# Optimization experiments

Hardware: AMD Instinct MI355X
Metric: run time of the kernel (lower is better)

Reference implementation:

```python
import jax, jax.numpy as jnp
import numpy as np

D_IN = 2048; D_OUT = 2048; DL = 512; NUM_HEAD = 16; CTX = 2048
HEAD_DIM = D_OUT // NUM_HEAD  # 128


def setup_inputs() -> dict:
    key = jax.random.key(0)
    ks = jax.random.split(key, 20)
    s = 0.02
    def lin(k, din, dout):
        k1, k2 = jax.random.split(k)
        return (jax.random.normal(k1, (din, dout), jnp.float32) * s,
                jax.random.normal(k2, (dout,), jnp.float32) * s)
    w_kv, b_kv = lin(ks[0], D_IN, DL)
    w_ku, b_ku = lin(ks[1], DL, D_OUT // 2)
    w_kr, b_kr = lin(ks[2], D_IN, D_OUT // 2)
    w_vu, b_vu = lin(ks[3], DL, D_OUT)
    w_q,  b_q  = lin(ks[4], D_IN, DL)
    w_qu, b_qu = lin(ks[5], DL, D_OUT // 2)
    w_qr, b_qr = lin(ks[6], DL, D_OUT // 2)
    w_o,  b_o  = lin(ks[7], D_OUT, D_OUT)
    x = jax.random.normal(ks[8], (2, 2048, D_IN), jnp.float32)
    return dict(x=x, w_kv=w_kv, b_kv=b_kv, w_ku=w_ku, b_ku=b_ku, w_kr=w_kr, b_kr=b_kr,
                w_vu=w_vu, b_vu=b_vu, w_q=w_q, b_q=b_q, w_qu=w_qu, b_qu=b_qu,
                w_qr=w_qr, b_qr=b_qr, w_o=w_o, b_o=b_o)


def reference(x, w_kv, b_kv, w_ku, b_ku, w_kr, b_kr, w_vu, b_vu,
              w_q, b_q, w_qu, b_qu, w_qr, b_qr, w_o, b_o):
    b, s, _ = x.shape
    # latent KV compression
    ckv = x @ w_kv + b_kv                                   # (b, s, dl)
    # NOTE: source Rope.forward is a no-op (returns input), replicated faithfully.
    key = jnp.concatenate([ckv @ w_ku + b_ku, x @ w_kr + b_kr], axis=-1)   # (b, s, d_out)
    q_lat = x @ w_q + b_q                                   # (b, s, dl)
    query = jnp.concatenate([q_lat @ w_qu + b_qu, q_lat @ w_qr + b_qr], axis=-1)
    value = ckv @ w_vu + b_vu                               # (b, s, d_out)
    # split heads -> (b, h, s, hd)
    def heads(t):
        return t.reshape(b, s, NUM_HEAD, HEAD_DIM).transpose(0, 2, 1, 3)
    q, k, v = heads(query), heads(key), heads(value)
    scores = jnp.einsum('bhqd,bhkd->bhqk', q, k)
    causal = jnp.tril(jnp.ones((s, s), dtype=bool))
    scores = jnp.where(causal, scores, -jnp.inf)
    at = jax.nn.softmax(scores / jnp.sqrt(jnp.float32(HEAD_DIM)), axis=-1)
    # dropout rate 0 -> identity
    out = jnp.einsum('bhqk,bhkd->bhqd', at, v).transpose(0, 2, 1, 3).reshape(b, s, D_OUT)
    return out @ w_o + b_o
```

## Files before the change

kernel.cpp:

```cpp
#include <hip/hip_runtime.h>
#include <hip/hip_bf16.h>

typedef __hip_bfloat16 bf16;
typedef __bf16 bf16_t;
typedef __bf16 bf16x8 __attribute__((ext_vector_type(8)));
typedef __bf16 bf16x4v __attribute__((ext_vector_type(4)));
typedef float f32x4 __attribute__((ext_vector_type(4)));

#define D_IN 2048
#define D_OUT 2048
#define DL 512
#define NUM_HEAD 16
#define SEQ 2048
#define HEAD_DIM 128
#define BATCH 2
#define NTOK (BATCH * SEQ)
#define SCALE 0.08838834764831845f

struct CTrue  { static constexpr bool value = true;  };
struct CFalse { static constexpr bool value = false; };

__device__ __forceinline__ void stf(float* p, float v) { *p = v; }
__device__ __forceinline__ void stf(bf16_t* p, float v) { *p = (bf16_t)v; }

__device__ __forceinline__ void async_cp16(const bf16_t* g, bf16_t* l) {
    __builtin_amdgcn_global_load_lds(
        (const __attribute__((address_space(1))) void*)g,
        (__attribute__((address_space(3))) void*)l, 16, 0, 0);
}

#define CVTB 8192
#define NTOPS 8

struct TOp { const float* W; bf16_t* Wt; int K, N, nx, nblk; };
struct TOps { TOp op[NTOPS]; };

__global__ __launch_bounds__(256) void prep_kernel(
    const float* __restrict__ x, bf16_t* __restrict__ xb,
    TOps ops,
    const float* __restrict__ b_kv, const float* __restrict__ b_q,
    float* __restrict__ bkvq,
    const float* __restrict__ b_qu, const float* __restrict__ b_qr,
    float* __restrict__ bquqr, int trb)
{
    const int tid = threadIdx.x;
    int blk = blockIdx.x;

    if (blk < CVTB) {
        int i = (blk * 256 + tid) * 4;
        float4 v = *(const float4*)&x[i];
        bf16_t o[4] = {(bf16_t)v.x, (bf16_t)v.y, (bf16_t)v.z, (bf16_t)v.w};
        *(ulong1*)&xb[i] = *(ulong1*)o;
        return;
    }
    blk -= CVTB;
    if (blk < trb) {
        int op = 0;
        while (blk >= ops.op[op].nblk) { blk -= ops.op[op].nblk; ++op; }
        const TOp& t = ops.op[op];
        const int n0 = (blk % t.nx) * 32, k0 = (blk / t.nx) * 32;
        __shared__ float tl[32][33];
        const int c = tid & 31, r0 = tid >> 5;
#pragma unroll
        for (int rr = 0; rr < 32; rr += 8)
            tl[r0 + rr][c] = t.W[(size_t)(k0 + r0 + rr) * t.N + n0 + c];
        __syncthreads();
#pragma unroll
        for (int rr = 0; rr < 32; rr += 8)
            t.Wt[(size_t)(n0 + r0 + rr) * t.K + k0 + c] = (bf16_t)tl[c][r0 + rr];
        return;
    }
    blk -= trb;
    if (blk == 0) {
#pragma unroll
        for (int j = 0; j < 4; ++j) {
            int i = tid + j * 256;
            bkvq[i] = (i < DL) ? b_kv[i] : b_q[i - DL];
        }
    } else {
#pragma unroll
        for (int j = 0; j < 8; ++j) {
            int i = tid + j * 256;
            bquqr[i] = (i < 1024) ? b_qu[i] : b_qr[i - 1024];
        }
    }
}

struct GOp { const bf16_t* A; const bf16_t* Wt; const float* bias;
             void* C; int lda, K, col0, ldc, nx, nblk; float cscale; };
template <int N> struct GOps { GOp op[N]; };

template <typename TC, int NOPS>
__global__ __launch_bounds__(256) void gemm_multi_kernel(GOps<NOPS> ops)
{
    __shared__ __align__(16) bf16_t As[2 * 128 * 32];
    __shared__ __align__(16) bf16_t Bs[2 * 128 * 32];

    int blk = blockIdx.x;
    int opi = 0;
    while (blk >= ops.op[opi].nblk) { blk -= ops.op[opi].nblk; ++opi; }
    const GOp& g = ops.op[opi];

    const int tid  = threadIdx.x;
    const int wave = tid >> 6, lane = tid & 63;
    const int quad = lane >> 4, l16 = lane & 15;
    const int wm = wave & 1, wn = wave >> 1;
    const int m0 = (blk / g.nx) * 128;
    const int n0 = (blk % g.nx) * 128;

    const int r0 = tid >> 2, c0 = (tid & 3) * 8;
    const bf16_t* Ap0 = g.A  + (size_t)(m0 + r0)      * g.lda + c0;
    const bf16_t* Ap1 = g.A  + (size_t)(m0 + r0 + 64) * g.lda + c0;
    const bf16_t* Bp0 = g.Wt + (size_t)(n0 + r0)      * g.K   + c0;
    const bf16_t* Bp1 = g.Wt + (size_t)(n0 + r0 + 64) * g.K   + c0;

    f32x4 acc[4][4];
#pragma unroll
    for (int i = 0; i < 4; ++i)
#pragma unroll
        for (int j = 0; j < 4; ++j) acc[i][j] = (f32x4){0.f, 0.f, 0.f, 0.f};

    for (int k0 = 0; k0 < g.K; k0 += 64) {
        __syncthreads();
#pragma unroll
        for (int p = 0; p < 2; ++p) {
            async_cp16(Ap0 + k0 + p * 32, As + p * 4096 + tid * 8);
            async_cp16(Ap1 + k0 + p * 32, As + p * 4096 + 2048 + tid * 8);
            async_cp16(Bp0 + k0 + p * 32, Bs + p * 4096 + tid * 8);
            async_cp16(Bp1 + k0 + p * 32, Bs + p * 4096 + 2048 + tid * 8);
        }
        __syncthreads();

#pragma unroll
        for (int p = 0; p < 2; ++p) {
            bf16x8 af[4], bfr[4];
#pragma unroll
            for (int t = 0; t < 4; ++t) {
                af[t]  = *(const bf16x8*)&As[p * 4096 + (wm * 64 + t * 16 + l16) * 32 + quad * 8];
                bfr[t] = *(const bf16x8*)&Bs[p * 4096 + (wn * 64 + t * 16 + l16) * 32 + quad * 8];
            }
#pragma unroll
            for (int mt = 0; mt < 4; ++mt)
#pragma unroll
                for (int nt = 0; nt < 4; ++nt)
                    acc[mt][nt] = __builtin_amdgcn_mfma_f32_16x16x32_bf16(
                        af[mt], bfr[nt], acc[mt][nt], 0, 0, 0);
        }
    }

    TC* C = (TC*)g.C;
    const int mrow = m0 + wm * 64 + quad * 4;
#pragma unroll
    for (int mt = 0; mt < 4; ++mt)
#pragma unroll
        for (int nt = 0; nt < 4; ++nt) {
            int col = n0 + wn * 64 + nt * 16 + l16;
            float bv = g.bias[col];
#pragma unroll
            for (int r = 0; r < 4; ++r)
                stf(&C[(size_t)(mrow + mt * 16 + r) * g.ldc + g.col0 + col],
                    (acc[mt][nt][r] + bv) * g.cscale);
        }
}

#define KS_LD 136
#define VT_LD 72
#define KS_SZ (64 * KS_LD)
#define VT_SZ (128 * VT_LD)

__global__ __launch_bounds__(256, 2) void attn_mfma_kernel(
    bf16_t* __restrict__ Qg, const bf16_t* __restrict__ Kg,
    const bf16_t* __restrict__ Vg)
{
    __shared__ __align__(16) bf16_t Ks[2][KS_SZ];
    __shared__ __align__(16) bf16_t Vt[2][VT_SZ];

    const int tid  = threadIdx.x;
    const int wave = tid >> 6;
    const int lane = tid & 63;
    const int quad = lane >> 4;
    const int l16  = lane & 15;

    const int grp = blockIdx.x & 31;
    const int h   = grp & 15;
    const int b   = grp >> 4;
    const int p   = blockIdx.x >> 5;
    const int qtA = p, qtB = 31 - p;
    const int ntiles = qtB + 1;

    const int base = b * SEQ;
    const int hd0  = h * HEAD_DIM;

    bf16x8 qfA[4], qfB[4];
    {
        const bf16_t* qa = Qg + (size_t)(base + qtA * 64 + wave * 16 + l16) * D_OUT + hd0;
        const bf16_t* qb = Qg + (size_t)(base + qtB * 64 + wave * 16 + l16) * D_OUT + hd0;
#pragma unroll
        for (int kb = 0; kb < 4; ++kb) {
            qfA[kb] = *(const bf16x8*)(qa + kb * 32 + quad * 8);
            qfB[kb] = *(const bf16x8*)(qb + kb * 32 + quad * 8);
        }
    }

    f32x4 oA[8], oB[8];
#pragma unroll
    for (int ob = 0; ob < 8; ++ob) {
        oA[ob] = (f32x4){0.f, 0.f, 0.f, 0.f};
        oB[ob] = (f32x4){0.f, 0.f, 0.f, 0.f};
    }
    float lA = 0.f, lB = 0.f;

    const int rk = tid >> 4, ck = (tid & 15) * 8;
    const int kg = (tid & 15) * 4, dg = tid >> 4;
    const int rbase = (rk >> 2) * 8 + (rk & 3);

    bf16x8 kpre[4], vpre[4];
    auto issue = [&](int k0) {
        const bf16_t* kp = Kg + (size_t)(base + k0 + rbase) * D_OUT + hd0 + ck;
        kpre[0] = *(const bf16x8*)(kp);
        kpre[1] = *(const bf16x8*)(kp + (size_t)4  * D_OUT);
        kpre[2] = *(const bf16x8*)(kp + (size_t)32 * D_OUT);
        kpre[3] = *(const bf16x8*)(kp + (size_t)36 * D_OUT);
#pragma unroll
        for (int kk = 0; kk < 4; ++kk)
            vpre[kk] = *(const bf16x8*)&Vg[(size_t)(base + k0 + kg + kk) * D_OUT + hd0 + dg * 8];
    };

    auto stage = [&](int buf) {
        bf16_t* ks = Ks[buf]; bf16_t* vt = Vt[buf];
#pragma unroll
        for (int jj = 0; jj < 4; ++jj)
            *(bf16x8*)&ks[(rk + 16 * jj) * KS_LD + ck] = kpre[jj];
#pragma unroll
        for (int j = 0; j < 8; ++j) {
            bf16x4v pk = {vpre[0][j], vpre[1][j], vpre[2][j], vpre[3][j]};
            *(bf16x4v*)&vt[(dg * 8 + j) * VT_LD + kg] = pk;
        }
    };

    const int qabsA = qtA * 64 + wave * 16 + l16;
    const int qabsB = qtB * 64 + wave * 16 + l16;
    const int qwavA = qtA * 64 + wave * 16;
    const int qwavB = qtB * 64 + wave * 16;

    auto softmax_one = [&](f32x4* s, float& l_i, bf16x8& pb0, bf16x8& pb1) {
#pragma unroll
        for (int nb = 0; nb < 4; ++nb)
#pragma unroll
            for (int r = 0; r < 4; ++r) s[nb][r] = __expf(s[nb][r]);
        float r0 = ((s[0][0] + s[0][1]) + (s[0][2] + s[0][3]))
                 + ((s[1][0] + s[1][1]) + (s[1][2] + s[1][3]));
        float r1 = ((s[2][0] + s[2][1]) + (s[2][2] + s[2][3]))
                 + ((s[3][0] + s[3][1]) + (s[3][2] + s[3][3]));
        l_i += r0 + r1;
#pragma unroll
        for (int r = 0; r < 4; ++r) {
            pb0[r]     = (bf16_t)s[0][r];
            pb0[4 + r] = (bf16_t)s[1][r];
            pb1[r]     = (bf16_t)s[2][r];
            pb1[4 + r] = (bf16_t)s[3][r];
        }
    };

    auto tile_body = [&](auto doa, int cur, int k0) {
        constexpr bool DOA = decltype(doa)::value;
        const bf16_t* ks = Ks[cur];
        const bf16_t* vt = Vt[cur];

        f32x4 sB[4], sA[4];
#pragma unroll
        for (int nb = 0; nb < 4; ++nb) {
            sB[nb] = (f32x4){0.f, 0.f, 0.f, 0.f};
            sA[nb] = (f32x4){0.f, 0.f, 0.f, 0.f};
        }

        __builtin_amdgcn_s_setprio(1);
#pragma unroll
        for (int kb = 0; kb < 4; ++kb)
#pragma unroll
            for (int nb = 0; nb < 4; ++nb) {
                bf16x8 kf = *(const bf16x8*)&ks[(nb * 16 + l16) * KS_LD + kb * 32 + quad * 8];
                sB[nb] = __builtin_amdgcn_mfma_f32_16x16x32_bf16(kf, qfB[kb], sB[nb], 0, 0, 0);
                if constexpr (DOA)
                    sA[nb] = __builtin_amdgcn_mfma_f32_16x16x32_bf16(kf, qfA[kb], sA[nb], 0, 0, 0);
            }
        __builtin_amdgcn_s_setprio(0);

        if (k0 + 63 > qwavB) {
#pragma unroll
            for (int nb = 0; nb < 4; ++nb) {
                int key = k0 + (nb >> 1) * 32 + quad * 8 + (nb & 1) * 4;
#pragma unroll
                for (int r = 0; r < 4; ++r)
                    if (key + r > qabsB) sB[nb][r] = -INFINITY;
            }
        }
        if constexpr (DOA) {
            if (k0 + 63 > qwavA) {
#pragma unroll
                for (int nb = 0; nb < 4; ++nb) {
                    int key = k0 + (nb >> 1) * 32 + quad * 8 + (nb & 1) * 4;
#pragma unroll
                    for (int r = 0; r < 4; ++r)
                        if (key + r > qabsA) sA[nb][r] = -INFINITY;
                }
            }
        }

        bf16x8 pbB0, pbB1, pbA0, pbA1;
        softmax_one(sB, lB, pbB0, pbB1);
        if constexpr (DOA) softmax_one(sA, lA, pbA0, pbA1);

        __builtin_amdgcn_s_setprio(1);
#pragma unroll
        for (int ob = 0; ob < 8; ++ob) {
            bf16x8 v0 = *(const bf16x8*)&vt[(ob * 16 + l16) * VT_LD + quad * 8];
            oB[ob] = __builtin_amdgcn_mfma_f32_16x16x32_bf16(v0, pbB0, oB[ob], 0, 0, 0);
            if constexpr (DOA)
                oA[ob] = __builtin_amdgcn_mfma_f32_16x16x32_bf16(v0, pbA0, oA[ob], 0, 0, 0);
            bf16x8 v1 = *(const bf16x8*)&vt[(ob * 16 + l16) * VT_LD + 32 + quad * 8];
            oB[ob] = __builtin_amdgcn_mfma_f32_16x16x32_bf16(v1, pbB1, oB[ob], 0, 0, 0);
            if constexpr (DOA)
                oA[ob] = __builtin_amdgcn_mfma_f32_16x16x32_bf16(v1, pbA1, oA[ob], 0, 0, 0);
        }
        __builtin_amdgcn_s_setprio(0);
    };

    issue(0);
    stage(0);
    issue(64);
    __syncthreads();

    for (int t = 0; t < ntiles; ++t) {
        const int k0 = t * 64;
        const int cur = t & 1;
        if (t + 1 < ntiles) {
            stage(cur ^ 1);
            if (t + 2 < ntiles) issue((t + 2) * 64);
        }
        if (t <= qtA) tile_body(CTrue{},  cur, k0);
        else          tile_body(CFalse{}, cur, k0);
        __syncthreads();
    }

    auto writeback = [&](f32x4* o, float l_i, int qt) {
        float ls = l_i + __shfl_xor(l_i, 16, 64);
        ls += __shfl_xor(ls, 32, 64);
        const int q = qt * 64 + wave * 16 + l16;
        const float inv = 1.f / ls;
        bf16_t* orow = Qg + (size_t)(base + q) * D_OUT + hd0;
#pragma unroll
        for (int ob = 0; ob < 8; ++ob) {
            bf16x4v pk = {(bf16_t)(o[ob][0] * inv), (bf16_t)(o[ob][1] * inv),
                          (bf16_t)(o[ob][2] * inv), (bf16_t)(o[ob][3] * inv)};
            *(bf16x4v*)&orow[ob * 16 + quad * 4] = pk;
        }
    };
    writeback(oA, lA, qtA);
    writeback(oB, lB, qtB);
}

extern "C" void kernel_launch(void* const* d_in, const int* in_sizes, int n_in,
                              void* d_out, int out_size, void* d_ws, size_t ws_size,
                              hipStream_t stream)
{
    const float* x    = (const float*)d_in[0];
    const float* w_kv = (const float*)d_in[1];
    const float* b_kv = (const float*)d_in[2];
    const float* w_ku = (const float*)d_in[3];
    const float* b_ku = (const float*)d_in[4];
    const float* w_kr = (const float*)d_in[5];
    const float* b_kr = (const float*)d_in[6];
    const float* w_vu = (const float*)d_in[7];
    const float* b_vu = (const float*)d_in[8];
    const float* w_q  = (const float*)d_in[9];
    const float* b_q  = (const float*)d_in[10];
    const float* w_qu = (const float*)d_in[11];
    const float* b_qu = (const float*)d_in[12];
    const float* w_qr = (const float*)d_in[13];
    const float* b_qr = (const float*)d_in[14];
    const float* w_o  = (const float*)d_in[15];
    const float* b_o  = (const float*)d_in[16];
    float* out = (float*)d_out;

    bf16_t* ws    = (bf16_t*)d_ws;
    bf16_t* ckvq  = ws;
    bf16_t* query = ckvq  + NTOK * 1024;
    bf16_t* value = query + NTOK * D_OUT;
    bf16_t* wt_kv = value + NTOK * D_OUT;
    bf16_t* wt_q  = wt_kv + 512 * 2048;
    bf16_t* wt_ku = wt_q  + 512 * 2048;
    bf16_t* wt_kr = wt_ku + 1024 * 512;
    bf16_t* wt_vu = wt_kr + 1024 * 2048;
    bf16_t* wt_qu = wt_vu + 2048 * 512;
    bf16_t* wt_qr = wt_qu + 1024 * 512;
    bf16_t* wt_o  = wt_qr + 1024 * 512;
    float*  bkvq  = (float*)(wt_o + 2048 * 2048);
    float*  bquqr = bkvq + 1024;
    bf16_t* key   = (bf16_t*)d_out;
    bf16_t* xb    = key + NTOK * D_OUT;

    TOps tops = {{
        { w_kv, wt_kv, 2048,  512, 16,  16 * 64 },
        { w_q,  wt_q,  2048,  512, 16,  16 * 64 },
        { w_ku, wt_ku,  512, 1024, 32,  32 * 16 },
        { w_kr, wt_kr, 2048, 1024, 32,  32 * 64 },
        { w_vu, wt_vu,  512, 2048, 64,  64 * 16 },
        { w_qu, wt_qu,  512, 1024, 32,  32 * 16 },
        { w_qr, wt_qr,  512, 1024, 32,  32 * 16 },
        { w_o,  wt_o,  2048, 2048, 64,  64 * 64 },
    }};
    int trb = 0;
    for (int i = 0; i < NTOPS; ++i) trb += tops.op[i].nblk;
    prep_kernel<<<CVTB + trb + 2, 256, 0, stream>>>(
        x, xb, tops, b_kv, b_q, bkvq, b_qu, b_qr, bquqr, trb);

    GOps<2> s1 = {{
        { xb, wt_kv, bkvq, ckvq, D_IN, D_IN,    0, 1024,  8, 256, 1.f },
        { xb, wt_kr, b_kr, key,  D_IN, 2048, 1024, D_OUT, 8, 256, 1.f },
    }};
    gemm_multi_kernel<bf16_t, 2><<<512, 256, 0, stream>>>(s1);

    GOps<3> s2 = {{
        { ckvq + 512, wt_qu, bquqr, query, 1024, 512, 0, D_OUT, 16, 512, SCALE },
        { ckvq,       wt_vu, b_vu,  value, 1024, 512, 0, D_OUT, 16, 512, 1.f   },
        { ckvq,       wt_ku, b_ku,  key,   1024, 512, 0, D_OUT,  8, 256, 1.f   },
    }};
    gemm_multi_kernel<bf16_t, 3><<<1280, 256, 0, stream>>>(s2);

    attn_mfma_kernel<<<512, 256, 0, stream>>>(query, key, value);

    GOps<1> s3 = {{
        { query, wt_o, b_o, out, D_OUT, 2048, 0, D_OUT, 16, 512, 1.f },
    }};
    gemm_multi_kernel<float, 1><<<512, 256, 0, stream>>>(s3);
}
```

Before: 327.9 us.

## Use 128x64 GEMM tiles for stage-1 and output GEMMs; vectorize weight transpose

Adds a BN template parameter to the multi-op GEMM so the stage-1 projection and output projection use 128x64 tiles. This doubles the block count from 512 to 1024 for better occupancy and CU fill on the many-CU GPU, at the cost of more A-tile reloads per output. The weight transpose in the prep kernel now uses float4 loads and packed 4xbf16 stores with a padded shared tile, which cuts the number of memory transactions.

```diff
diff --git a/kernel.cpp b/kernel.cpp
--- a/kernel.cpp
+++ b/kernel.cpp
@@ -59,15 +59,15 @@
         while (blk >= ops.op[op].nblk) { blk -= ops.op[op].nblk; ++op; }
         const TOp& t = ops.op[op];
         const int n0 = (blk % t.nx) * 32, k0 = (blk / t.nx) * 32;
-        __shared__ float tl[32][33];
-        const int c = tid & 31, r0 = tid >> 5;
-#pragma unroll
-        for (int rr = 0; rr < 32; rr += 8)
-            tl[r0 + rr][c] = t.W[(size_t)(k0 + r0 + rr) * t.N + n0 + c];
+        __shared__ float tl[32][36];
+        const int r  = tid >> 3;
+        const int cb = (tid & 7) * 4;
+        float4 v = *(const float4*)&t.W[(size_t)(k0 + r) * t.N + n0 + cb];
+        *(float4*)&tl[r][cb] = v;
         __syncthreads();
-#pragma unroll
-        for (int rr = 0; rr < 32; rr += 8)
-            t.Wt[(size_t)(n0 + r0 + rr) * t.K + k0 + c] = (bf16_t)tl[c][r0 + rr];
+        bf16_t o[4] = {(bf16_t)tl[cb + 0][r], (bf16_t)tl[cb + 1][r],
+                       (bf16_t)tl[cb + 2][r], (bf16_t)tl[cb + 3][r]};
+        *(ulong1*)&t.Wt[(size_t)(n0 + r) * t.K + k0 + cb] = *(ulong1*)o;
         return;
     }
     blk -= trb;
@@ -90,11 +90,13 @@
              void* C; int lda, K, col0, ldc, nx, nblk; float cscale; };
 template <int N> struct GOps { GOp op[N]; };
 
-template <typename TC, int NOPS>
+template <typename TC, int NOPS, int BN>
 __global__ __launch_bounds__(256) void gemm_multi_kernel(GOps<NOPS> ops)
 {
+    constexpr int NT   = BN / 32;
+    constexpr int BSZP = BN * 32;
     __shared__ __align__(16) bf16_t As[2 * 128 * 32];
-    __shared__ __align__(16) bf16_t Bs[2 * 128 * 32];
+    __shared__ __align__(16) bf16_t Bs[2 * BSZP];
 
     int blk = blockIdx.x;
     int opi = 0;
@@ -106,7 +108,7 @@
     const int quad = lane >> 4, l16 = lane & 15;
     const int wm = wave & 1, wn = wave >> 1;
     const int m0 = (blk / g.nx) * 128;
-    const int n0 = (blk % g.nx) * 128;
+    const int n0 = (blk % g.nx) * BN;
 
     const int r0 = tid >> 2, c0 = (tid & 3) * 8;
     const bf16_t* Ap0 = g.A  + (size_t)(m0 + r0)      * g.lda + c0;
@@ -114,11 +116,11 @@
     const bf16_t* Bp0 = g.Wt + (size_t)(n0 + r0)      * g.K   + c0;
     const bf16_t* Bp1 = g.Wt + (size_t)(n0 + r0 + 64) * g.K   + c0;
 
-    f32x4 acc[4][4];
+    f32x4 acc[4][NT];
 #pragma unroll
     for (int i = 0; i < 4; ++i)
 #pragma unroll
-        for (int j = 0; j < 4; ++j) acc[i][j] = (f32x4){0.f, 0.f, 0.f, 0.f};
+        for (int j = 0; j < NT; ++j) acc[i][j] = (f32x4){0.f, 0.f, 0.f, 0.f};
 
     for (int k0 = 0; k0 < g.K; k0 += 64) {
         __syncthreads();
@@ -126,23 +128,25 @@
         for (int p = 0; p < 2; ++p) {
             async_cp16(Ap0 + k0 + p * 32, As + p * 4096 + tid * 8);
             async_cp16(Ap1 + k0 + p * 32, As + p * 4096 + 2048 + tid * 8);
-            async_cp16(Bp0 + k0 + p * 32, Bs + p * 4096 + tid * 8);
-            async_cp16(Bp1 + k0 + p * 32, Bs + p * 4096 + 2048 + tid * 8);
+            async_cp16(Bp0 + k0 + p * 32, Bs + p * BSZP + tid * 8);
+            if constexpr (BN == 128)
+                async_cp16(Bp1 + k0 + p * 32, Bs + p * BSZP + 2048 + tid * 8);
         }
         __syncthreads();
 
 #pragma unroll
         for (int p = 0; p < 2; ++p) {
-            bf16x8 af[4], bfr[4];
-#pragma unroll
-            for (int t = 0; t < 4; ++t) {
-                af[t]  = *(const bf16x8*)&As[p * 4096 + (wm * 64 + t * 16 + l16) * 32 + quad * 8];
-                bfr[t] = *(const bf16x8*)&Bs[p * 4096 + (wn * 64 + t * 16 + l16) * 32 + quad * 8];
-            }
+            bf16x8 af[4], bfr[NT];
+#pragma unroll
+            for (int t = 0; t < 4; ++t)
+                af[t] = *(const bf16x8*)&As[p * 4096 + (wm * 64 + t * 16 + l16) * 32 + quad * 8];
+#pragma unroll
+            for (int t = 0; t < NT; ++t)
+                bfr[t] = *(const bf16x8*)&Bs[p * BSZP + (wn * (BN / 2) + t * 16 + l16) * 32 + quad * 8];
 #pragma unroll
             for (int mt = 0; mt < 4; ++mt)
 #pragma unroll
-                for (int nt = 0; nt < 4; ++nt)
+                for (int nt = 0; nt < NT; ++nt)
                     acc[mt][nt] = __builtin_amdgcn_mfma_f32_16x16x32_bf16(
                         af[mt], bfr[nt], acc[mt][nt], 0, 0, 0);
         }
@@ -153,8 +157,8 @@
 #pragma unroll
     for (int mt = 0; mt < 4; ++mt)
 #pragma unroll
-        for (int nt = 0; nt < 4; ++nt) {
-            int col = n0 + wn * 64 + nt * 16 + l16;
+        for (int nt = 0; nt < NT; ++nt) {
+            int col = n0 + wn * (BN / 2) + nt * 16 + l16;
             float bv = g.bias[col];
 #pragma unroll
             for (int r = 0; r < 4; ++r)
@@ -416,22 +420,22 @@
         x, xb, tops, b_kv, b_q, bkvq, b_qu, b_qr, bquqr, trb);
 
     GOps<2> s1 = {{
-        { xb, wt_kv, bkvq, ckvq, D_IN, D_IN,    0, 1024,  8, 256, 1.f },
-        { xb, wt_kr, b_kr, key,  D_IN, 2048, 1024, D_OUT, 8, 256, 1.f },
+        { xb, wt_kv, bkvq, ckvq, D_IN, D_IN,    0, 1024, 16, 512, 1.f },
+        { xb, wt_kr, b_kr, key,  D_IN, 2048, 1024, D_OUT, 16, 512, 1.f },
     }};
-    gemm_multi_kernel<bf16_t, 2><<<512, 256, 0, stream>>>(s1);
+    gemm_multi_kernel<bf16_t, 2, 64><<<1024, 256, 0, stream>>>(s1);
 
     GOps<3> s2 = {{
         { ckvq + 512, wt_qu, bquqr, query, 1024, 512, 0, D_OUT, 16, 512, SCALE },
         { ckvq,       wt_vu, b_vu,  value, 1024, 512, 0, D_OUT, 16, 512, 1.f   },
         { ckvq,       wt_ku, b_ku,  key,   1024, 512, 0, D_OUT,  8, 256, 1.f   },
     }};
-    gemm_multi_kernel<bf16_t, 3><<<1280, 256, 0, stream>>>(s2);
+    gemm_multi_kernel<bf16_t, 3, 128><<<1280, 256, 0, stream>>>(s2);
 
     attn_mfma_kernel<<<512, 256, 0, stream>>>(query, key, value);
 
     GOps<1> s3 = {{
-        { query, wt_o, b_o, out, D_OUT, 2048, 0, D_OUT, 16, 512, 1.f },
+        { query, wt_o, b_o, out, D_OUT, 2048, 0, D_OUT, 32, 1024, 1.f },
     }};
-    gemm_multi_kernel<float, 1><<<512, 256, 0, stream>>>(s3);
+    gemm_multi_kernel<float, 1, 64><<<1024, 256, 0, stream>>>(s3);
 }
```

After: 343.2 us. 1.05x slower.
